# Kernel optimization log

Hardware: AMD Instinct MI355X
Metric: run time of the kernel (lower is better)

Reference implementation:

```python
import jax, jax.numpy as jnp
import numpy as np

N_SUBJECTS = 16
N_LABELS = 8
DENS_TEMP = 0.1  # args.ProtoSim_dens_temp


def setup_inputs() -> dict:
    key = jax.random.key(0)
    k1, k2, k3 = jax.random.split(key, 3)
    B, C, D = 16384, 2, 1024
    X_data = jax.random.normal(k1, (B, C, D), dtype=jnp.float32)
    subject = jax.random.randint(k2, (B,), 0, N_SUBJECTS, dtype=jnp.int64) if jax.config.jax_enable_x64 else jax.random.randint(k2, (B,), 0, N_SUBJECTS).astype(jnp.int32)
    labels = jax.random.randint(k3, (B,), 0, N_LABELS).astype(subject.dtype)
    return {"X_data": X_data, "subject": subject, "labels": labels}


def reference(X_data, subject, labels):
    B, C, D = X_data.shape
    K = N_SUBJECTS * N_LABELS  # all (subject,label) groups assumed present
    # contrast_feature = cat(unbind(X_data, 1), 0) -> [B*C, D]
    feat = X_data.swapaxes(0, 1).reshape(B * C, D)
    sub2 = jnp.tile(subject, C)          # cat((subject, subject))
    lab2 = jnp.tile(labels, C)
    # torch.unique sorts -> group g = subject * N_LABELS + label matches loop order
    gid = sub2 * N_LABELS + lab2
    counts = jax.ops.segment_sum(jnp.ones((B * C,), feat.dtype), gid, num_segments=K)  # (K,)
    centroid = jax.ops.segment_sum(feat, gid, num_segments=K) / counts[:, None]       # (K, D)
    # per-row euclidean distance to own group centroid (torch.cdist to 1 point)
    dist = jnp.linalg.norm(feat - centroid[gid], axis=1)                               # (B*C,)
    mean_sqrt = jax.ops.segment_sum(jnp.sqrt(dist), gid, num_segments=K) / counts
    density = mean_sqrt / jnp.log(counts + 10.0)
    density = jnp.where(counts <= 1.0, density.max(), density)
    density = jnp.clip(density, jnp.quantile(density, 0.1), jnp.quantile(density, 0.9))
    density = DENS_TEMP * density / density.mean()                                     # (K,)
    # masks: positives = same label, different subject
    g_sub = jnp.arange(K) // N_LABELS
    g_lab = jnp.arange(K) % N_LABELS
    subj_mask = (sub2[:, None] != g_sub[None, :]).astype(feat.dtype)  # (B*C, K)
    lab_mask = (lab2[:, None] == g_lab[None, :]).astype(feat.dtype)
    mask = subj_mask * lab_mask
    # every row has N_SUBJECTS-1 positives (all groups present), so no row filtering
    sim = (feat @ centroid.T) / density[None, :]                                        # (B*C, K)
    sim = sim - sim.max(axis=1, keepdims=True)
    pos = sim * mask
    logp = jax.nn.log_softmax(pos, axis=1)
    row_loss = -(mask * logp).sum(axis=1) / mask.sum(axis=1)  # soft-target CE / #pos
    return row_loss.reshape(C, B).mean()
```

## Files before the change

### kernel.cpp

```cpp
#include <hip/hip_runtime.h>
#include <hip/hip_bf16.h>
#include <math.h>

#define NSUB 16
#define NLAB 8
#define KG 128
#define BN 16384
#define DD 1024

typedef float v4f __attribute__((ext_vector_type(4)));
typedef short short8v __attribute__((ext_vector_type(8)));
typedef unsigned short ushort4v __attribute__((ext_vector_type(4)));

static __device__ __forceinline__ short f2bf(float f) {
    unsigned u = __builtin_bit_cast(unsigned, f);
    unsigned r = (u + 0x7fffu + ((u >> 16) & 1u)) >> 16;
    return (short)r;
}

static __device__ __forceinline__ float bf2f(unsigned short u) {
    unsigned v = ((unsigned)u) << 16;
    return __builtin_bit_cast(float, v);
}

static __device__ __forceinline__ unsigned packbf2(float x, float y) {
    union { __hip_bfloat162 h; unsigned u; } c;
    c.h = __float22bfloat162_rn(float2{x, y});
    return c.u;
}

__global__ __launch_bounds__(1024) void k0_gid(const int* __restrict__ subject,
                                               const int* __restrict__ labels,
                                               int* __restrict__ gid, int* __restrict__ hist) {
    __shared__ int h[KG];
    int t = threadIdx.x;
    if (t < KG) h[t] = 0;
    __syncthreads();
    int b = blockIdx.x * 1024 + t;
    int g = subject[b] * NLAB + labels[b];
    gid[b] = g;
    atomicAdd(&h[g], 1);
    __syncthreads();
    if (t < KG) hist[blockIdx.x * KG + t] = h[t];
}

__global__ __launch_bounds__(1024) void k0c_scatter(const int* __restrict__ gid,
                                                    const int* __restrict__ hist,
                                                    int* __restrict__ cnt,
                                                    int* __restrict__ rowlist) {
    __shared__ int tots[KG], base0[KG], lcur[KG];
    int t = threadIdx.x, bi = blockIdx.x;
    if (t < KG) {
        int tot = 0, pre = 0;
#pragma unroll
        for (int j = 0; j < 16; ++j) {
            int v = hist[j * KG + t];
            tot += v;
            if (j < bi) pre += v;
        }
        tots[t] = tot;
        base0[t] = pre;
        lcur[t] = 0;
        if (bi == 0) cnt[t] = tot;
    }
    __syncthreads();
    if (t < KG) {
        int o = 0;
        for (int j = 0; j < t; ++j) o += tots[j];
        base0[t] += o;
    }
    __syncthreads();
    int b = bi * 1024 + t;
    int g = gid[b];
    rowlist[base0[g] + atomicAdd(&lcur[g], 1)] = b;
}

__global__ __launch_bounds__(256) void k1_centroid(const float* __restrict__ X,
                                                   const int* __restrict__ rowlist,
                                                   const int* __restrict__ cnt,
                                                   unsigned short* __restrict__ Btil,
                                                   float* __restrict__ cnormPart,
                                                   unsigned short* __restrict__ Atil) {
    int g = blockIdx.x >> 1;
    int half = blockIdx.x & 1;
    int t = threadIdx.x, lane = t & 63, w = t >> 6;
    int d = half * 512 + t * 2;
    int kc = d >> 5, q = (d >> 3) & 3, jj = d & 7;
    int base_t = kc * 512 + q * 128 + jj;
    __shared__ int rows[512];
    __shared__ int sh_no[2];
    __shared__ float wsum[4];
    if (w == 0) {
        int v = 0;
        if (lane < g) v += cnt[lane];
        if (lane + 64 < g) v += cnt[lane + 64];
#pragma unroll
        for (int x = 32; x; x >>= 1) v += __shfl_xor(v, x, 64);
        if (lane == 0) { sh_no[0] = v; sh_no[1] = cnt[g]; }
    }
    __syncthreads();
    int o = sh_no[0], n = min(sh_no[1], 512);
    for (int i = t; i < n; i += 256) rows[i] = rowlist[o + i];
    __syncthreads();
    float ax = 0.f, ay = 0.f;
    int i = 0;
    for (; i + 16 <= n; i += 16) {
        float2 v[32];
        int rb[16];
#pragma unroll
        for (int u = 0; u < 16; ++u) {
            rb[u] = rows[i + u];
            size_t base = (size_t)rb[u] * 2048 + d;
            v[2 * u] = *(const float2*)(X + base);
            v[2 * u + 1] = *(const float2*)(X + base + 1024);
        }
#pragma unroll
        for (int u = 0; u < 16; ++u) {
            ax += v[2 * u].x + v[2 * u + 1].x;
            ay += v[2 * u].y + v[2 * u + 1].y;
            size_t rm = (size_t)(rb[u] >> 4) * 16384 + (size_t)(rb[u] & 15) * 8;
            *(unsigned*)(Atil + rm + base_t) = packbf2(v[2 * u].x, v[2 * u].y);
            *(unsigned*)(Atil + rm + 16777216 + base_t) = packbf2(v[2 * u + 1].x, v[2 * u + 1].y);
        }
    }
    for (; i < n; ++i) {
        int b = rows[i];
        size_t base = (size_t)b * 2048 + d;
        float2 v0 = *(const float2*)(X + base);
        float2 v1 = *(const float2*)(X + base + 1024);
        ax += v0.x + v1.x; ay += v0.y + v1.y;
        size_t rm = (size_t)(b >> 4) * 16384 + (size_t)(b & 15) * 8;
        *(unsigned*)(Atil + rm + base_t) = packbf2(v0.x, v0.y);
        *(unsigned*)(Atil + rm + 16777216 + base_t) = packbf2(v1.x, v1.y);
    }
    float inv = 1.f / (2.f * (float)n);
    float cx = ax * inv, cy = ay * inv;
    int gt = g >> 4, mc = g & 15;
    *(unsigned*)(Btil + (size_t)gt * 16384 + mc * 8 + base_t) = packbf2(cx, cy);
    float s = cx * cx + cy * cy;
#pragma unroll
    for (int x = 32; x; x >>= 1) s += __shfl_xor(s, x, 64);
    if (lane == 0) wsum[w] = s;
    __syncthreads();
    if (t == 0) cnormPart[half * KG + g] = wsum[0] + wsum[1] + wsum[2] + wsum[3];
}

__global__ __launch_bounds__(256) void k5a_dot(const unsigned short* __restrict__ Atil,
                                               const unsigned short* __restrict__ Btil,
                                               const int* __restrict__ gid,
                                               const float* __restrict__ cnormPart,
                                               unsigned short* __restrict__ Dotb,
                                               float* __restrict__ sqsPart) {
    __shared__ float h[KG];
    __shared__ float cnormS[KG];
    int t = threadIdx.x, lane = t & 63;
    if (t < KG) {
        h[t] = 0.f;
        cnormS[t] = cnormPart[t] + cnormPart[KG + t];
    }
    __syncthreads();
    int gw = blockIdx.x * 4 + (t >> 6);
    int row0 = gw * 32;
    int m = lane & 15, q = lane >> 4;
    const unsigned short* a0 = Atil + (size_t)(gw * 2) * 16384 + lane * 8;
    const unsigned short* a1 = a0 + 16384;
    const unsigned short* bb = Btil + lane * 8;

    v4f acc[2][8];
#pragma unroll
    for (int i = 0; i < 2; ++i)
#pragma unroll
        for (int j = 0; j < 8; ++j) acc[i][j] = (v4f){0.f, 0.f, 0.f, 0.f};

    short8v A0[4], A1[4], Bf[4][8];
#pragma unroll
    for (int p = 0; p < 4; ++p) {
        A0[p] = *(const short8v*)(a0 + p * 512);
        A1[p] = *(const short8v*)(a1 + p * 512);
#pragma unroll
        for (int gt = 0; gt < 8; ++gt)
            Bf[p][gt] = *(const short8v*)(bb + (size_t)gt * 16384 + p * 512);
    }
    float s0 = 0.f, s1 = 0.f;
#pragma unroll
    for (int kc = 0; kc < 32; ++kc) {
        const int cur = kc & 3;
        short8v nA0, nA1, nB[8];
        if (kc + 4 < 32) {
            nA0 = *(const short8v*)(a0 + (kc + 4) * 512);
            nA1 = *(const short8v*)(a1 + (kc + 4) * 512);
#pragma unroll
            for (int gt = 0; gt < 8; ++gt)
                nB[gt] = *(const short8v*)(bb + (size_t)gt * 16384 + (kc + 4) * 512);
        }
#pragma unroll
        for (int gt = 0; gt < 8; ++gt) {
            acc[0][gt] = __builtin_amdgcn_mfma_f32_16x16x32_bf16(A0[cur], Bf[cur][gt], acc[0][gt], 0, 0, 0);
            acc[1][gt] = __builtin_amdgcn_mfma_f32_16x16x32_bf16(A1[cur], Bf[cur][gt], acc[1][gt], 0, 0, 0);
        }
        {
            union { short8v s; unsigned u[4]; } ua, ub;
            ua.s = A0[cur]; ub.s = A1[cur];
#pragma unroll
            for (int r = 0; r < 4; ++r) {
                float l0 = __builtin_bit_cast(float, ua.u[r] << 16);
                float h0 = __builtin_bit_cast(float, ua.u[r] & 0xffff0000u);
                s0 = fmaf(l0, l0, s0); s0 = fmaf(h0, h0, s0);
                float l1 = __builtin_bit_cast(float, ub.u[r] << 16);
                float h1 = __builtin_bit_cast(float, ub.u[r] & 0xffff0000u);
                s1 = fmaf(l1, l1, s1); s1 = fmaf(h1, h1, s1);
            }
        }
        if (kc + 4 < 32) {
            A0[cur] = nA0; A1[cur] = nA1;
#pragma unroll
            for (int gt = 0; gt < 8; ++gt) Bf[cur][gt] = nB[gt];
        }
    }

    s0 += __shfl_xor(s0, 16, 64); s0 += __shfl_xor(s0, 32, 64);
    s1 += __shfl_xor(s1, 16, 64); s1 += __shfl_xor(s1, 32, 64);

    int rowblk = row0 >> 6, rlo = row0 & 32;
#pragma unroll
    for (int tile = 0; tile < 2; ++tile)
#pragma unroll
        for (int reg = 0; reg < 4; ++reg) {
            int rr = rlo + tile * 16 + q * 4 + reg;
            int row = (rowblk << 6) + rr;
            int b = row & (BN - 1);
            int g = gid[b];
            float own = 0.f;
#pragma unroll
            for (int gt = 0; gt < 8; ++gt) {
                float v = acc[tile][gt][reg];
                size_t idx = (((size_t)rowblk * 32 + gt * 4 + (m >> 2)) * 64 + rr) * 4 + (m & 3);
                Dotb[idx] = (unsigned short)f2bf(v);
                if ((g >> 4) == gt) own = v;
            }
            float rn = __shfl(tile ? s1 : s0, q * 4 + reg, 64);
            if ((g & 15) == m) {
                float d2 = fmaxf(rn - 2.f * own + cnormS[g], 0.f);
                atomicAdd(&h[g], sqrtf(sqrtf(d2)));
            }
        }
    __syncthreads();
    if (t < KG) sqsPart[(size_t)blockIdx.x * KG + t] = h[t];
}

__global__ __launch_bounds__(128) void k5b_loss(const unsigned short* __restrict__ Dotb,
                                                const int* __restrict__ gid,
                                                const float* __restrict__ sqsPart,
                                                const int* __restrict__ cnt,
                                                float* __restrict__ out) {
    __shared__ float tmp[KG], d1s[KG], qv[4];
    __shared__ float recipDen[KG];
    __shared__ float wsum[2];
    int t = threadIdx.x;
    float cntf = 0.f, d0v = 0.f, v = 0.f;
    if (t < KG) {
        float ss = 0.f;
        for (int j = 0; j < 256; j += 4)
            ss += sqsPart[(size_t)j * KG + t] + sqsPart[(size_t)(j + 1) * KG + t] +
                  sqsPart[(size_t)(j + 2) * KG + t] + sqsPart[(size_t)(j + 3) * KG + t];
        cntf = 2.f * (float)cnt[t];
        d0v = (ss / cntf) / logf(cntf + 10.f);
        tmp[t] = d0v;
    }
    __syncthreads();
    if (t < KG) {
        float dmax = -INFINITY;
        for (int j = 0; j < KG; ++j) dmax = fmaxf(dmax, tmp[j]);
        v = (cntf <= 1.f) ? dmax : d0v;
        d1s[t] = v;
    }
    __syncthreads();
    if (t < KG) {
        int less = 0, eq = 0;
        for (int j = 0; j < KG; ++j) {
            float u = d1s[j];
            less += (u < v) ? 1 : 0;
            eq += (u == v) ? 1 : 0;
        }
        const int ppos[4] = {12, 13, 114, 115};
        for (int qq = 0; qq < 4; ++qq)
            if (less <= ppos[qq] && ppos[qq] < less + eq) qv[qq] = v;
    }
    __syncthreads();
    if (t < KG) {
        float q10 = 0.3f * qv[0] + 0.7f * qv[1];
        float q90 = 0.7f * qv[2] + 0.3f * qv[3];
        tmp[t] = fminf(fmaxf(v, q10), q90);
    }
    __syncthreads();
    if (t < KG) {
        float sum = 0.f;
        for (int j = 0; j < KG; ++j) sum += tmp[j];
        float mean = sum / (float)KG;
        recipDen[t] = mean / (0.1f * tmp[t]);
    }
    __syncthreads();
    int row = blockIdx.x * 128 + t;
    int b = row & (BN - 1);
    int g = gid[b];
    int s = g >> 3, l = g & 7;
    int lane = t & 63, w = t >> 6;
    size_t rowblk = (size_t)(row >> 6);
    const ushort4v* dp = (const ushort4v*)Dotb;
    float mx = -INFINITY;
    float psave[16];
#pragma unroll
    for (int c = 0; c < 16; ++c) {
        size_t i0 = (rowblk * 32 + c * 2) * 64 + lane;
        ushort4v dv0 = dp[i0];
        ushort4v dv1 = dp[i0 + 64];
        const float* rv = &recipDen[c * 8];
        float x[8];
#pragma unroll
        for (int j = 0; j < 4; ++j) x[j] = bf2f((unsigned short)dv0[j]) * rv[j];
#pragma unroll
        for (int j = 0; j < 4; ++j) x[4 + j] = bf2f((unsigned short)dv1[j]) * rv[4 + j];
#pragma unroll
        for (int j = 0; j < 8; ++j) mx = fmaxf(mx, x[j]);
        float sel = x[0];
#pragma unroll
        for (int j = 1; j < 8; ++j) sel = (j == l) ? x[j] : sel;
        psave[c] = sel;
    }
    float S = 0.f, P = 0.f;
#pragma unroll
    for (int j = 0; j < 16; ++j) {
        float pv = psave[j] - mx;
        float e = expf(pv);
        bool use = (j != s);
        S += use ? e : 0.f;
        P += use ? pv : 0.f;
    }
    float ll = logf(113.f + S) - P * (1.f / 15.f);
#pragma unroll
    for (int x2 = 32; x2; x2 >>= 1) ll += __shfl_xor(ll, x2, 64);
    if (lane == 0) wsum[w] = ll;
    __syncthreads();
    if (t == 0) atomicAdd(out, (wsum[0] + wsum[1]) * (1.f / 32768.f));
}

extern "C" void kernel_launch(void* const* d_in, const int* in_sizes, int n_in,
                              void* d_out, int out_size, void* d_ws, size_t ws_size,
                              hipStream_t stream) {
    const float* X = (const float*)d_in[0];
    const int* subject = (const int*)d_in[1];
    const int* labels = (const int*)d_in[2];
    float* out = (float*)d_out;
    char* w = (char*)d_ws;
    int* gid = (int*)(w + 0);
    int* hist = (int*)(w + 65536);
    int* cnt = (int*)(w + 73728);
    float* cnormPart = (float*)(w + 74240);
    int* rowlist = (int*)(w + 131072);
    float* sqsPart = (float*)(w + 262144);
    unsigned short* Btil = (unsigned short*)(w + 524288);
    unsigned short* Atil = (unsigned short*)(w + 2097152);
    unsigned short* Dotb = (unsigned short*)(w + 100663296);

    (void)hipMemsetAsync(out, 0, sizeof(float), stream);

    k0_gid<<<16, 1024, 0, stream>>>(subject, labels, gid, hist);
    k0c_scatter<<<16, 1024, 0, stream>>>(gid, hist, cnt, rowlist);
    k1_centroid<<<KG * 2, 256, 0, stream>>>(X, rowlist, cnt, Btil, cnormPart, Atil);
    k5a_dot<<<256, 256, 0, stream>>>(Atil, Btil, gid, cnormPart, Dotb, sqsPart);
    k5b_loss<<<256, 128, 0, stream>>>(Dotb, gid, sqsPart, cnt, out);
}
```

Before: 296.7 us.

## Split bf16 tiled-A conversion out of centroid kernel into coalesced LDS-staged kernel

The centroid kernel no longer writes the bf16 tiled copy of X with scattered 4-byte stores. A new kernel reads X row-tiles with float4 loads, packs them to bf16 in swizzled shared memory, and writes the tiled layout with 16-byte coalesced stores. This targets the uncoalesced scattered-store cost in the centroid pass. The price is a second full read of X (128 MB) and an extra launch.

After: 261.3 us. 1.14x faster.

```diff
diff --git a/kernel.cpp b/kernel.cpp
--- a/kernel.cpp
+++ b/kernel.cpp
@@ -79,8 +79,7 @@
                                                    const int* __restrict__ rowlist,
                                                    const int* __restrict__ cnt,
                                                    unsigned short* __restrict__ Btil,
-                                                   float* __restrict__ cnormPart,
-                                                   unsigned short* __restrict__ Atil) {
+                                                   float* __restrict__ cnormPart) {
     int g = blockIdx.x >> 1;
     int half = blockIdx.x & 1;
     int t = threadIdx.x, lane = t & 63, w = t >> 6;
@@ -106,32 +105,20 @@
     int i = 0;
     for (; i + 16 <= n; i += 16) {
         float2 v[32];
-        int rb[16];
 #pragma unroll
         for (int u = 0; u < 16; ++u) {
-            rb[u] = rows[i + u];
-            size_t base = (size_t)rb[u] * 2048 + d;
+            size_t base = (size_t)rows[i + u] * 2048 + d;
             v[2 * u] = *(const float2*)(X + base);
             v[2 * u + 1] = *(const float2*)(X + base + 1024);
         }
 #pragma unroll
-        for (int u = 0; u < 16; ++u) {
-            ax += v[2 * u].x + v[2 * u + 1].x;
-            ay += v[2 * u].y + v[2 * u + 1].y;
-            size_t rm = (size_t)(rb[u] >> 4) * 16384 + (size_t)(rb[u] & 15) * 8;
-            *(unsigned*)(Atil + rm + base_t) = packbf2(v[2 * u].x, v[2 * u].y);
-            *(unsigned*)(Atil + rm + 16777216 + base_t) = packbf2(v[2 * u + 1].x, v[2 * u + 1].y);
-        }
+        for (int u = 0; u < 32; ++u) { ax += v[u].x; ay += v[u].y; }
     }
     for (; i < n; ++i) {
-        int b = rows[i];
-        size_t base = (size_t)b * 2048 + d;
+        size_t base = (size_t)rows[i] * 2048 + d;
         float2 v0 = *(const float2*)(X + base);
         float2 v1 = *(const float2*)(X + base + 1024);
         ax += v0.x + v1.x; ay += v0.y + v1.y;
-        size_t rm = (size_t)(b >> 4) * 16384 + (size_t)(b & 15) * 8;
-        *(unsigned*)(Atil + rm + base_t) = packbf2(v0.x, v0.y);
-        *(unsigned*)(Atil + rm + 16777216 + base_t) = packbf2(v1.x, v1.y);
     }
     float inv = 1.f / (2.f * (float)n);
     float cx = ax * inv, cy = ay * inv;
@@ -143,6 +130,42 @@
     if (lane == 0) wsum[w] = s;
     __syncthreads();
     if (t == 0) cnormPart[half * KG + g] = wsum[0] + wsum[1] + wsum[2] + wsum[3];
+}
+
+__global__ __launch_bounds__(256) void k2_tile(const float* __restrict__ X,
+                                               unsigned short* __restrict__ Atil) {
+    __shared__ unsigned lds[8192];
+    int t = threadIdx.x, lane = t & 63, w = t >> 6;
+    int rt = blockIdx.x;
+#pragma unroll
+    for (int p = 0; p < 4; ++p) {
+        int m = w * 4 + p;
+        int r = rt * 16 + m;
+        const float* xp = X + (size_t)(r & (BN - 1)) * 2048 + (size_t)(r >> 14) * 1024;
+        unsigned swz = (unsigned)((m & 7) << 2);
+        unsigned mbase = (unsigned)m * 512;
+#pragma unroll
+        for (int j = 0; j < 4; ++j) {
+            int d0 = j * 256 + lane * 4;
+            float4 v = *(const float4*)(xp + d0);
+            unsigned wi = mbase + (((unsigned)(d0 >> 1)) ^ swz);
+            lds[wi] = packbf2(v.x, v.y);
+            lds[wi + 1] = packbf2(v.z, v.w);
+        }
+    }
+    __syncthreads();
+    size_t gbase = (size_t)rt * 16384;
+#pragma unroll
+    for (int p = 0; p < 8; ++p) {
+        int wo = p * 1024 + t * 4;
+        int kc = wo >> 8;
+        int q = (wo >> 6) & 3;
+        int m = (wo >> 2) & 15;
+        unsigned wi = (unsigned)m * 512 +
+                      (((unsigned)(kc * 16 + q * 4)) ^ (unsigned)((m & 7) << 2));
+        uint4 val = *(const uint4*)&lds[wi];
+        *(uint4*)(Atil + gbase + (size_t)wo * 2) = val;
+    }
 }
 
 __global__ __launch_bounds__(256) void k5a_dot(const unsigned short* __restrict__ Atil,
@@ -366,7 +389,8 @@
 
     k0_gid<<<16, 1024, 0, stream>>>(subject, labels, gid, hist);
     k0c_scatter<<<16, 1024, 0, stream>>>(gid, hist, cnt, rowlist);
-    k1_centroid<<<KG * 2, 256, 0, stream>>>(X, rowlist, cnt, Btil, cnormPart, Atil);
+    k1_centroid<<<KG * 2, 256, 0, stream>>>(X, rowlist, cnt, Btil, cnormPart);
+    k2_tile<<<2048, 256, 0, stream>>>(X, Atil);
     k5a_dot<<<256, 256, 0, stream>>>(Atil, Btil, gid, cnormPart, Dotb, sqsPart);
     k5b_loss<<<256, 128, 0, stream>>>(Dotb, gid, sqsPart, cnt, out);
 }
```
